# Optimization experiments

Measured on AMD Instinct MI355X. Metric: run time of the kernel, lower is better.

Reference implementation:

```python
import jax, jax.numpy as jnp
import numpy as np


def _next_power2(n: int) -> int:
    return 1 << (n - 1).bit_length()


def setup_inputs() -> dict:
    key = jax.random.key(0)
    k1, k2, k3 = jax.random.split(key, 3)
    N, C, W = 32, 8, 65536
    F, WW = 16, 64
    x = jax.random.normal(k1, (N, C, W), dtype=jnp.float32)
    w = jax.random.normal(k2, (F, C, WW), dtype=jnp.float32)
    b = jax.random.normal(k3, (F,), dtype=jnp.float32)
    return {"x": x, "w": w, "b": b}


def reference(x, w, b):
    # FFT-based 1D cross-correlation (valid mode), no spectral compression
    # (preserve_energy_rate=index_back=out_size=padding=None).
    N, C, W = x.shape
    F, _, WW = w.shape
    out_W = W - WW + 1
    fftsize = _next_power2(W + WW - 1)
    Xf = jnp.fft.rfft(x, fftsize)                     # (N, C, Fr) complex
    Wf = jnp.fft.rfft(w, fftsize)                     # (F, C, Fr) complex
    # correlation = irfft(X * conj(W)); sum over channels C
    prod = jnp.einsum("ncf,kcf->nkf", Xf, jnp.conj(Wf))  # (N, F, Fr)
    out = jnp.fft.irfft(prod, fftsize)[..., :out_W]      # (N, F, out_W)
    # Original code adds bias[ff] inside the channel loop -> bias added C times.
    return out + (C * b)[None, :, None]
```

## Files before the change

### kernel.cpp

```cpp
#include <hip/hip_runtime.h>
#include <stdint.h>

typedef _Float16 half8 __attribute__((ext_vector_type(8)));
typedef __fp16 fp16x2 __attribute__((ext_vector_type(2)));
typedef float f32x4 __attribute__((ext_vector_type(4)));
typedef float f32x2 __attribute__((ext_vector_type(2)));
typedef uint32_t u32x2 __attribute__((ext_vector_type(2)));

#define N_ 32
#define C_ 8
#define W_ 65536
#define F_ 16
#define OW_ 65473
#define K_ 512
#define TILE_T 1024
#define XS 1152

__device__ __forceinline__ uint32_t funnel16(uint32_t hi, uint32_t lo) {
  return (uint32_t)((((uint64_t)hi << 32) | (uint64_t)lo) >> 16);
}

__device__ __forceinline__ uint32_t pk(float a, float b) {
  union { fp16x2 h; uint32_t u; } cv;
  cv.h = __builtin_amdgcn_cvt_pkrtz(a, b);
  return cv.u;
}

__device__ __forceinline__ uint32_t wswz(uint32_t e) {
  uint32_t ch = e >> 3;
  ch ^= (ch >> 6) & 7u;
  return (ch << 4) | ((e & 7u) << 1);
}

__device__ __forceinline__ f32x4 ldx(const float* p) {
  return *reinterpret_cast<const f32x4*>(p);
}

template<bool TAIL>
__device__ __forceinline__ void block_job(const float* __restrict__ x,
                                          const float* __restrict__ w,
                                          const float* __restrict__ b,
                                          float* __restrict__ out,
                                          _Float16* wl, _Float16* xb,
                                          int n, int t0) {
  const int tid  = threadIdx.x;
  const int lane = tid & 63;
  const int wv   = tid >> 6;
  const int c15  = lane & 15;
  const int g    = lane >> 4;

  const float* xn = x + (size_t)n * (C_ * W_);

  #pragma unroll
  for (int j = 0; j < 4; ++j) {
    int e = (tid + 512 * j) * 4;
    f32x4 v = ldx(w + e);
    u32x2 p; p[0] = pk(v[0], v[1]); p[1] = pk(v[2], v[3]);
    *reinterpret_cast<u32x2*>(reinterpret_cast<char*>(wl) + wswz((uint32_t)e)) = p;
  }

  #pragma unroll
  for (int j = 0; j < 5; ++j) {
    int u = tid + 512 * j;
    if (j == 4 && u >= 2176) break;
    int ch = u / 272;
    int pos = (u - ch * 272) * 4;
    int gi = t0 + pos;
    f32x4 v;
    if (TAIL) v = (gi < W_) ? ldx(xn + (size_t)ch * W_ + gi) : (f32x4){0.f,0.f,0.f,0.f};
    else      v = ldx(xn + (size_t)ch * W_ + gi);
    u32x2 p; p[0] = pk(v[0], v[1]); p[1] = pk(v[2], v[3]);
    *reinterpret_cast<u32x2*>(reinterpret_cast<char*>(xb) + (size_t)(ch * XS + pos) * 2u) = p;
  }

  const f32x4 bv = *reinterpret_cast<const f32x4*>(b + 4 * g);

  __syncthreads();

  const int tlw = wv << 7;

  f32x4 acc[8];
  #pragma unroll
  for (int r = 0; r < 8; ++r) acc[r] = (f32x4){0.f, 0.f, 0.f, 0.f};

  union Win { half8 h[2]; uint32_t d[8]; };

  #pragma unroll
  for (int s = 0; s < 16; ++s) {
    const uint32_t we = (uint32_t)(c15 * K_ + 32 * s + 8 * g);
    const half8 wf = *reinterpret_cast<const half8*>(
                         reinterpret_cast<const char*>(wl) + wswz(we));
    const int c  = s >> 1;
    const int jb = (s & 1) * 32;
    const int A0 = tlw + 8 * c15 + jb + 8 * g;
    Win win;
    win.h[0] = *reinterpret_cast<const half8*>(xb + c * XS + A0);
    win.h[1] = *reinterpret_cast<const half8*>(xb + c * XS + A0 + 8);
    #pragma unroll
    for (int r = 0; r < 8; ++r) {
      union { uint32_t d[4]; half8 h; } fr;
      const int m = r >> 1;
      if ((r & 1) == 0) {
        fr.d[0] = win.d[m];     fr.d[1] = win.d[m + 1];
        fr.d[2] = win.d[m + 2]; fr.d[3] = win.d[m + 3];
      } else {
        fr.d[0] = funnel16(win.d[m + 1], win.d[m]);
        fr.d[1] = funnel16(win.d[m + 2], win.d[m + 1]);
        fr.d[2] = funnel16(win.d[m + 3], win.d[m + 2]);
        fr.d[3] = funnel16(win.d[m + 4], win.d[m + 3]);
      }
      acc[r] = __builtin_amdgcn_mfma_f32_16x16x32_f16(wf, fr.h, acc[r], 0, 0, 0);
    }
  }

  const int T = t0 + tlw + 8 * c15;
  float* outn = out + (size_t)n * F_ * OW_;
  #pragma unroll
  for (int q = 0; q < 4; ++q) {
    const float bias = 8.0f * bv[q];
    float sv[8];
    #pragma unroll
    for (int j = 0; j < 8; ++j) sv[j] = acc[j][q] + bias;
    float* row = outn + (size_t)(4 * g + q) * OW_ + T;
    if (!TAIL || T + 8 <= OW_) {
      if (q == 0) {
        *reinterpret_cast<f32x4*>(row)     = (f32x4){sv[0], sv[1], sv[2], sv[3]};
        *reinterpret_cast<f32x4*>(row + 4) = (f32x4){sv[4], sv[5], sv[6], sv[7]};
      } else if (q == 2) {
        *reinterpret_cast<f32x2*>(row)     = (f32x2){sv[0], sv[1]};
        *reinterpret_cast<f32x2*>(row + 2) = (f32x2){sv[2], sv[3]};
        *reinterpret_cast<f32x2*>(row + 4) = (f32x2){sv[4], sv[5]};
        *reinterpret_cast<f32x2*>(row + 6) = (f32x2){sv[6], sv[7]};
      } else {
        row[0] = sv[0];
        *reinterpret_cast<f32x2*>(row + 1) = (f32x2){sv[1], sv[2]};
        *reinterpret_cast<f32x2*>(row + 3) = (f32x2){sv[3], sv[4]};
        *reinterpret_cast<f32x2*>(row + 5) = (f32x2){sv[5], sv[6]};
        row[7] = sv[7];
      }
    } else {
      #pragma unroll
      for (int j = 0; j < 8; ++j) if (T + j < OW_) row[j] = sv[j];
    }
  }
}

__global__ __launch_bounds__(512, 6)
void corr1d(const float* __restrict__ x, const float* __restrict__ w,
            const float* __restrict__ b, float* __restrict__ out) {
  __shared__ __align__(16) _Float16 wl[F_ * K_];
  __shared__ __align__(16) _Float16 xb[C_ * XS];

  const int n  = blockIdx.x >> 6;
  const int tt = blockIdx.x & 63;
  const int t0 = tt * TILE_T;

  if (tt < 63) block_job<false>(x, w, b, out, wl, xb, n, t0);
  else         block_job<true >(x, w, b, out, wl, xb, n, t0);
}

extern "C" void kernel_launch(void* const* d_in, const int* in_sizes, int n_in,
                              void* d_out, int out_size, void* d_ws, size_t ws_size,
                              hipStream_t stream) {
  (void)in_sizes; (void)n_in; (void)out_size; (void)d_ws; (void)ws_size;
  const float* x = (const float*)d_in[0];
  const float* w = (const float*)d_in[1];
  const float* b = (const float*)d_in[2];
  float* out = (float*)d_out;
  corr1d<<<dim3(32 * 64), dim3(512), 0, stream>>>(x, w, b, out);
}
```

Measured before the change: 53.01 us.

## Process two time tiles per block with double-buffered x prefetch overlapping MFMA

```diff
diff --git a/kernel.cpp b/kernel.cpp
--- a/kernel.cpp
+++ b/kernel.cpp
@@ -15,6 +15,7 @@
 #define K_ 512
 #define TILE_T 1024
 #define XS 1152
+#define XBUF (C_ * XS)
 
 __device__ __forceinline__ uint32_t funnel16(uint32_t hi, uint32_t lo) {
   return (uint32_t)((((uint64_t)hi << 32) | (uint64_t)lo) >> 16);
@@ -36,57 +37,48 @@
   return *reinterpret_cast<const f32x4*>(p);
 }
 
-template<bool TAIL>
-__device__ __forceinline__ void block_job(const float* __restrict__ x,
-                                          const float* __restrict__ w,
-                                          const float* __restrict__ b,
-                                          float* __restrict__ out,
-                                          _Float16* wl, _Float16* xb,
-                                          int n, int t0) {
-  const int tid  = threadIdx.x;
-  const int lane = tid & 63;
-  const int wv   = tid >> 6;
-  const int c15  = lane & 15;
-  const int g    = lane >> 4;
-
-  const float* xn = x + (size_t)n * (C_ * W_);
-
-  #pragma unroll
-  for (int j = 0; j < 4; ++j) {
-    int e = (tid + 512 * j) * 4;
-    f32x4 v = ldx(w + e);
-    u32x2 p; p[0] = pk(v[0], v[1]); p[1] = pk(v[2], v[3]);
-    *reinterpret_cast<u32x2*>(reinterpret_cast<char*>(wl) + wswz((uint32_t)e)) = p;
-  }
-
-  #pragma unroll
-  for (int j = 0; j < 5; ++j) {
-    int u = tid + 512 * j;
-    if (j == 4 && u >= 2176) break;
-    int ch = u / 272;
-    int pos = (u - ch * 272) * 4;
-    int gi = t0 + pos;
-    f32x4 v;
-    if (TAIL) v = (gi < W_) ? ldx(xn + (size_t)ch * W_ + gi) : (f32x4){0.f,0.f,0.f,0.f};
-    else      v = ldx(xn + (size_t)ch * W_ + gi);
-    u32x2 p; p[0] = pk(v[0], v[1]); p[1] = pk(v[2], v[3]);
-    *reinterpret_cast<u32x2*>(reinterpret_cast<char*>(xb) + (size_t)(ch * XS + pos) * 2u) = p;
-  }
-
-  const f32x4 bv = *reinterpret_cast<const f32x4*>(b + 4 * g);
-
-  __syncthreads();
-
-  const int tlw = wv << 7;
-
-  f32x4 acc[8];
-  #pragma unroll
-  for (int r = 0; r < 8; ++r) acc[r] = (f32x4){0.f, 0.f, 0.f, 0.f};
-
+__device__ __forceinline__ f32x4 xunit_load(const float* __restrict__ xn,
+                                            int t0, int u, bool guard) {
+  int ch = u / 272;
+  int pos = (u - ch * 272) * 4;
+  int gi = t0 + pos;
+  if (guard && gi >= W_) return (f32x4){0.f, 0.f, 0.f, 0.f};
+  return ldx(xn + (size_t)ch * W_ + gi);
+}
+
+__device__ __forceinline__ void xunit_write(_Float16* __restrict__ xb,
+                                            int u, f32x4 v) {
+  int ch = u / 272;
+  int pos = (u - ch * 272) * 4;
+  u32x2 p; p[0] = pk(v[0], v[1]); p[1] = pk(v[2], v[3]);
+  *reinterpret_cast<u32x2*>(reinterpret_cast<char*>(xb) +
+                            (size_t)(ch * XS + pos) * 2u) = p;
+}
+
+__device__ __forceinline__ void xload_half(const float* __restrict__ xn, int t0,
+                                           int tid, bool guard, int h,
+                                           f32x4 pre[3]) {
+  const int ub = h * 1088;
+  pre[0] = xunit_load(xn, t0, ub + tid, guard);
+  pre[1] = xunit_load(xn, t0, ub + 512 + tid, guard);
+  if (tid < 64) pre[2] = xunit_load(xn, t0, ub + 1024 + tid, guard);
+}
+
+__device__ __forceinline__ void xwrite_half(_Float16* __restrict__ xb, int tid,
+                                            int h, const f32x4 pre[3]) {
+  const int ub = h * 1088;
+  xunit_write(xb, ub + tid, pre[0]);
+  xunit_write(xb, ub + 512 + tid, pre[1]);
+  if (tid < 64) xunit_write(xb, ub + 1024 + tid, pre[2]);
+}
+
+template<int S0>
+__device__ __forceinline__ void khalf(const _Float16* __restrict__ wl,
+                                      const _Float16* __restrict__ xb,
+                                      f32x4 acc[8], int c15, int g, int tlw) {
   union Win { half8 h[2]; uint32_t d[8]; };
-
-  #pragma unroll
-  for (int s = 0; s < 16; ++s) {
+  #pragma unroll
+  for (int s = S0; s < S0 + 8; ++s) {
     const uint32_t we = (uint32_t)(c15 * K_ + 32 * s + 8 * g);
     const half8 wf = *reinterpret_cast<const half8*>(
                          reinterpret_cast<const char*>(wl) + wswz(we));
@@ -112,9 +104,12 @@
       acc[r] = __builtin_amdgcn_mfma_f32_16x16x32_f16(wf, fr.h, acc[r], 0, 0, 0);
     }
   }
-
-  const int T = t0 + tlw + 8 * c15;
-  float* outn = out + (size_t)n * F_ * OW_;
+}
+
+template<bool GUARD>
+__device__ __forceinline__ void epilogue(const f32x4 acc[8], f32x4 bv,
+                                         float* __restrict__ outn,
+                                         int T, int g) {
   #pragma unroll
   for (int q = 0; q < 4; ++q) {
     const float bias = 8.0f * bv[q];
@@ -122,7 +117,7 @@
     #pragma unroll
     for (int j = 0; j < 8; ++j) sv[j] = acc[j][q] + bias;
     float* row = outn + (size_t)(4 * g + q) * OW_ + T;
-    if (!TAIL || T + 8 <= OW_) {
+    if (!GUARD || T + 8 <= OW_) {
       if (q == 0) {
         *reinterpret_cast<f32x4*>(row)     = (f32x4){sv[0], sv[1], sv[2], sv[3]};
         *reinterpret_cast<f32x4*>(row + 4) = (f32x4){sv[4], sv[5], sv[6], sv[7]};
@@ -145,18 +140,82 @@
   }
 }
 
+template<bool TAIL>
+__device__ __forceinline__ void block_job(const float* __restrict__ x,
+                                          const float* __restrict__ w,
+                                          const float* __restrict__ b,
+                                          float* __restrict__ out,
+                                          _Float16* wl, _Float16* xb0,
+                                          _Float16* xb1, int n, int tb0) {
+  const int tid  = threadIdx.x;
+  const int lane = tid & 63;
+  const int wv   = tid >> 6;
+  const int c15  = lane & 15;
+  const int g    = lane >> 4;
+  const int tlw  = wv << 7;
+
+  const float* xn = x + (size_t)n * (C_ * W_);
+  float* outn = out + (size_t)n * F_ * OW_;
+
+  #pragma unroll
+  for (int j = 0; j < 4; ++j) {
+    int e = (tid + 512 * j) * 4;
+    f32x4 v = ldx(w + e);
+    u32x2 p; p[0] = pk(v[0], v[1]); p[1] = pk(v[2], v[3]);
+    *reinterpret_cast<u32x2*>(reinterpret_cast<char*>(wl) + wswz((uint32_t)e)) = p;
+  }
+
+  {
+    f32x4 p0[3], p1[3];
+    xload_half(xn, tb0, tid, false, 0, p0);
+    xload_half(xn, tb0, tid, false, 1, p1);
+    xwrite_half(xb0, tid, 0, p0);
+    xwrite_half(xb0, tid, 1, p1);
+  }
+
+  const f32x4 bv = *reinterpret_cast<const f32x4*>(b + 4 * g);
+
+  __syncthreads();
+
+  f32x4 acc[8];
+  #pragma unroll
+  for (int r = 0; r < 8; ++r) acc[r] = (f32x4){0.f, 0.f, 0.f, 0.f};
+
+  const int t0B = tb0 + TILE_T;
+  f32x4 pre[3];
+
+  xload_half(xn, t0B, tid, TAIL, 0, pre);
+  khalf<0>(wl, xb0, acc, c15, g, tlw);
+  xwrite_half(xb1, tid, 0, pre);
+  xload_half(xn, t0B, tid, TAIL, 1, pre);
+  khalf<8>(wl, xb0, acc, c15, g, tlw);
+  xwrite_half(xb1, tid, 1, pre);
+
+  __syncthreads();
+
+  epilogue<false>(acc, bv, outn, tb0 + tlw + 8 * c15, g);
+
+  #pragma unroll
+  for (int r = 0; r < 8; ++r) acc[r] = (f32x4){0.f, 0.f, 0.f, 0.f};
+
+  khalf<0>(wl, xb1, acc, c15, g, tlw);
+  khalf<8>(wl, xb1, acc, c15, g, tlw);
+
+  epilogue<TAIL>(acc, bv, outn, t0B + tlw + 8 * c15, g);
+}
+
 __global__ __launch_bounds__(512, 6)
 void corr1d(const float* __restrict__ x, const float* __restrict__ w,
             const float* __restrict__ b, float* __restrict__ out) {
   __shared__ __align__(16) _Float16 wl[F_ * K_];
-  __shared__ __align__(16) _Float16 xb[C_ * XS];
-
-  const int n  = blockIdx.x >> 6;
-  const int tt = blockIdx.x & 63;
-  const int t0 = tt * TILE_T;
-
-  if (tt < 63) block_job<false>(x, w, b, out, wl, xb, n, t0);
-  else         block_job<true >(x, w, b, out, wl, xb, n, t0);
+  __shared__ __align__(16) _Float16 xb[2][XBUF];
+
+  const int n  = blockIdx.x >> 5;
+  const int bt = blockIdx.x & 31;
+  const int tb0 = bt << 11;
+
+  if (bt < 31) block_job<false>(x, w, b, out, wl, xb[0], xb[1], n, tb0);
+  else         block_job<true >(x, w, b, out, wl, xb[0], xb[1], n, tb0);
 }
 
 extern "C" void kernel_launch(void* const* d_in, const int* in_sizes, int n_in,
@@ -167,5 +226,5 @@
   const float* w = (const float*)d_in[1];
   const float* b = (const float*)d_in[2];
   float* out = (float*)d_out;
-  corr1d<<<dim3(32 * 64), dim3(512), 0, stream>>>(x, w, b, out);
-}
+  corr1d<<<dim3(32 * 32), dim3(512), 0, stream>>>(x, w, b, out);
+}
```

Result: slower. 73.23 us (+38.1%).
